# Optimization experiments

Measured on AMD Instinct MI355X. Metric: run time of the kernel, lower is better.

## Reference

```python
import jax, jax.numpy as jnp
import numpy as np

N = 131072
MUL = 64  # multiplicity of each irrep in x
FAN_IN = 128  # 2*MUL input channels per output irrep block
INV_SQRT_FAN = float(1.0 / np.sqrt(FAN_IN))
INV_SQRT3 = float(1.0 / np.sqrt(3.0))


def setup_inputs() -> dict:
    key = jax.random.key(0)
    k1, k2, k3, k4 = jax.random.split(key, 4)
    x = jax.random.normal(k1, (N, MUL + MUL * 3), dtype=jnp.float32)   # 64x0e + 64x1o
    y = jax.random.normal(k2, (N, 1 + 3), dtype=jnp.float32)           # 1x0e + 1x1o
    W0 = jax.random.normal(k3, (FAN_IN, 2 * MUL), dtype=jnp.float32)   # 0e block: 128 -> (64 gates + 64 scalars)
    b0 = jnp.zeros((2 * MUL,), dtype=jnp.float32)                      # bias only on scalars (0e)
    W1 = jax.random.normal(k4, (FAN_IN, MUL), dtype=jnp.float32)       # 1o block: 128 -> 64
    return {"x": x, "y": y, "W0": W0, "b0": b0, "W1": W1}


def reference(x, y, W0, b0, W1):
    # unpack irreps: x = 64x0e + 64x1o ; y = 1x0e + 1x1o
    x0 = x[:, :MUL]                       # [N, 64]
    x1 = x[:, MUL:].reshape(-1, MUL, 3)   # [N, 64, 3]
    y0 = y[:, :1]                         # [N, 1]
    y1 = y[:, 1:]                         # [N, 3]
    # Clebsch-Gordan tensor product (component normalization):
    #   0e x 0e -> 0e : x0 * y0
    #   1o x 1o -> 0e : dot(x1, y1)/sqrt(3)
    #   0e x 1o -> 1o : x0 * y1
    #   1o x 0e -> 1o : x1 * y0
    # (1e/2e paths are dropped by the Linear to 128x0e + 64x1o)
    tp0 = jnp.concatenate(
        [x0 * y0, jnp.einsum("nci,ni->nc", x1, y1) * INV_SQRT3], axis=-1
    )  # [N, 128] of 0e
    tp1 = jnp.concatenate(
        [x0[:, :, None] * y1[:, None, :], x1 * y0[:, :, None]], axis=1
    )  # [N, 128, 3] of 1o
    # irrep-wise Linear (element normalization => scale 1/sqrt(fan_in); bias on scalars)
    s = tp0 @ W0 * INV_SQRT_FAN + b0                      # [N, 128]: 64 gates + 64 scalars
    v = jnp.einsum("nci,co->noi", tp1, W1) * INV_SQRT_FAN  # [N, 64, 3]
    # gate: gelu on even scalars, sigmoid gates multiply the vectors
    gates = jax.nn.sigmoid(s[:, :MUL])
    scalars = jax.nn.gelu(s[:, MUL:])
    vec = (gates[:, :, None] * v).reshape(-1, MUL * 3)
    return jnp.concatenate([scalars, vec], axis=-1)  # [N, 256] = 64x0e + 64x1o
```

## Files before the change

### kernel.cpp

```cpp
#include <hip/hip_runtime.h>
#include <cstdint>

#define TPB 256

static constexpr float INV_SQRT_FAN = 0.08838834764831845f;
static constexpr float INV_SQRT3_C  = 0.5773502691896258f;

typedef _Float16 f16x4v __attribute__((ext_vector_type(4)));
typedef float f32x4 __attribute__((ext_vector_type(4)));

__device__ __align__(16) uint16_t g_wf[24576];

__device__ __forceinline__ uint16_t f2h(float f) {
  union { _Float16 h; uint16_t u; } cv;
  cv.h = (_Float16)f;
  return cv.u;
}
__device__ __forceinline__ uint32_t pk2(float a, float b) {
  return (uint32_t)f2h(a) | ((uint32_t)f2h(b) << 16);
}

__global__ void prep_kernel(const float* __restrict__ W0,
                            const float* __restrict__ W1) {
  int id = blockIdx.x * TPB + threadIdx.x;
  if (id < 16384) {
    int k = id >> 7, n = id & 127;
    g_wf[n * 128 + k] = f2h(W0[id]);
  } else {
    int i2 = id - 16384;
    int k = i2 >> 6, o = i2 & 63;
    g_wf[16384 + o * 128 + k] = f2h(W1[i2]);
  }
}

#define MFMA16H(a, b, c) __builtin_amdgcn_mfma_f32_16x16x16f16((a), (b), (c), 0, 0, 0)

__global__ __launch_bounds__(256, 4) void tplg_mfma(
    const float* __restrict__ x, const float* __restrict__ y,
    const float* __restrict__ b0, float* __restrict__ out) {
  __shared__ uint16_t lds16[18688];
  float* ldsf = (float*)lds16;
  float* s_stage = ldsf + 4096;
  float* v_stage = ldsf + 6208;

  const int t = threadIdx.x;
  const long rowBase = (long)blockIdx.x * 16;

  {
    const int u = t & 15;
    const int r = t >> 4;
    const float* xr = x + (rowBase + r) * 256;
    const float4 x0 = *(const float4*)(xr + 4 * u);
    const float4 aa = *(const float4*)(xr + 64 + 12 * u);
    const float4 bb = *(const float4*)(xr + 64 + 12 * u + 4);
    const float4 cc = *(const float4*)(xr + 64 + 12 * u + 8);
    const float4 yv = *(const float4*)(y + (rowBase + r) * 4);
    const float y0 = yv.x, y1 = yv.y, y2 = yv.z, y3 = yv.w;
    const float t0x = aa.x, t0y = aa.y, t0z = aa.z;
    const float t1x = aa.w, t1y = bb.x, t1z = bb.y;
    const float t2x = bb.z, t2y = bb.w, t2z = cc.x;
    const float t3x = cc.y, t3y = cc.z, t3z = cc.w;
    const int base = r * 512;
    const int us = u ^ r;
    *(uint2*)(lds16 + base + us * 4) =
        make_uint2(pk2(x0.x * y0, x0.y * y0), pk2(x0.z * y0, x0.w * y0));
    const float d0 = (t0x * y1 + t0y * y2 + t0z * y3) * INV_SQRT3_C;
    const float d1 = (t1x * y1 + t1y * y2 + t1z * y3) * INV_SQRT3_C;
    const float d2 = (t2x * y1 + t2y * y2 + t2z * y3) * INV_SQRT3_C;
    const float d3 = (t3x * y1 + t3y * y2 + t3z * y3) * INV_SQRT3_C;
    *(uint2*)(lds16 + base + (16 + us) * 4) = make_uint2(pk2(d0, d1), pk2(d2, d3));
    *(uint2*)(lds16 + base + (32 + us) * 4) =
        make_uint2(pk2(x0.x * y1, x0.y * y1), pk2(x0.z * y1, x0.w * y1));
    *(uint2*)(lds16 + base + (48 + us) * 4) =
        make_uint2(pk2(t0x * y0, t1x * y0), pk2(t2x * y0, t3x * y0));
    *(uint2*)(lds16 + base + (64 + us) * 4) =
        make_uint2(pk2(x0.x * y2, x0.y * y2), pk2(x0.z * y2, x0.w * y2));
    *(uint2*)(lds16 + base + (80 + us) * 4) =
        make_uint2(pk2(t0y * y0, t1y * y0), pk2(t2y * y0, t3y * y0));
    *(uint2*)(lds16 + base + (96 + us) * 4) =
        make_uint2(pk2(x0.x * y3, x0.y * y3), pk2(x0.z * y3, x0.w * y3));
    *(uint2*)(lds16 + base + (112 + us) * 4) =
        make_uint2(pk2(t0z * y0, t1z * y0), pk2(t2z * y0, t3z * y0));
  }
  __syncthreads();

  {
    const int wave = t >> 6;
    const int lane = t & 63;
    const int g = lane >> 4;
    const int q = lane & 15;
    const f32x4 zf = {0.f, 0.f, 0.f, 0.f};

    if (wave < 2) {
      const int nb = wave * 64;
      f32x4 p[4] = {zf, zf, zf, zf};
      const uint16_t* tpr = lds16 + q * 512;
      #pragma unroll
      for (int m2 = 0; m2 < 8; ++m2) {
        const f16x4v a = *(const f16x4v*)(tpr + ((m2 * 4 + g) ^ q) * 4);
        #pragma unroll
        for (int nt = 0; nt < 4; ++nt) {
          const f16x4v b =
              *(const f16x4v*)(g_wf + (nb + nt * 16 + q) * 128 + m2 * 16 + g * 4);
          p[nt] = MFMA16H(a, b, p[nt]);
        }
      }
      #pragma unroll
      for (int nt = 0; nt < 4; ++nt)
        #pragma unroll
        for (int j = 0; j < 4; ++j)
          s_stage[(g * 4 + j) * 132 + nb + nt * 16 + q] = p[nt][j];
    } else {
      const int ob = (wave - 2) * 32;
      f32x4 acc[2][3] = {{zf, zf, zf}, {zf, zf, zf}};
      #pragma unroll
      for (int m2 = 0; m2 < 8; ++m2) {
        f16x4v av[3];
        #pragma unroll
        for (int i = 0; i < 3; ++i)
          av[i] = *(const f16x4v*)(lds16 + q * 512 +
                                   (((1 + i) * 32 + m2 * 4 + g) ^ q) * 4);
        #pragma unroll
        for (int nt = 0; nt < 2; ++nt) {
          const f16x4v b = *(const f16x4v*)(g_wf + 16384 +
                                            (ob + nt * 16 + q) * 128 + m2 * 16 + g * 4);
          #pragma unroll
          for (int i = 0; i < 3; ++i) acc[nt][i] = MFMA16H(av[i], b, acc[nt][i]);
        }
      }
      #pragma unroll
      for (int nt = 0; nt < 2; ++nt)
        #pragma unroll
        for (int i = 0; i < 3; ++i)
          #pragma unroll
          for (int j = 0; j < 4; ++j)
            v_stage[(g * 4 + j) * 196 + (ob + nt * 16 + q) * 3 + i] = acc[nt][i][j];
    }
  }
  __syncthreads();

  const int r = t >> 4, w = t & 15;
  float sacc[8], vacc[12];
  #pragma unroll
  for (int n = 0; n < 8; ++n) sacc[n] = s_stage[r * 132 + 8 * w + n];
  #pragma unroll
  for (int o4 = 0; o4 < 4; ++o4)
    #pragma unroll
    for (int i = 0; i < 3; ++i)
      vacc[o4 * 3 + i] = v_stage[r * 196 + (4 * w + o4) * 3 + i];
  __syncthreads();

  float* gatep = ldsf;
  float* stg   = ldsf + 1024;
  if (w < 8) {
    #pragma unroll
    for (int n = 0; n < 8; ++n) {
      const int col = 8 * w + n;
      const float s = sacc[n] * INV_SQRT_FAN + b0[col];
      gatep[r * 64 + col] = __builtin_amdgcn_rcpf(1.0f + __expf(-s));
    }
  } else {
    #pragma unroll
    for (int n = 0; n < 8; ++n) {
      const int col = 8 * w + n;
      const float s = sacc[n] * INV_SQRT_FAN + b0[col];
      const float u3 = s * s * s;
      const float ua = 0.7978845608028654f * (s + 0.044715f * u3);
      const float e = __expf(2.0f * ua);
      const float th = 1.0f - 2.0f * __builtin_amdgcn_rcpf(e + 1.0f);
      stg[r * 256 + (col - 64)] = 0.5f * s * (1.0f + th);
    }
  }
  __syncthreads();
  #pragma unroll
  for (int o4 = 0; o4 < 4; ++o4) {
    const int o = 4 * w + o4;
    const float gq = gatep[r * 64 + o];
    #pragma unroll
    for (int i = 0; i < 3; ++i) {
      stg[r * 256 + 64 + o * 3 + i] = gq * vacc[o4 * 3 + i] * INV_SQRT_FAN;
    }
  }
  __syncthreads();

  const float4* s4 = (const float4*)stg;
  float4* o4p = (float4*)(out + rowBase * 256);
  #pragma unroll
  for (int i = 0; i < 4; ++i) o4p[i * 256 + t] = s4[i * 256 + t];
}

extern "C" void kernel_launch(void* const* d_in, const int* in_sizes, int n_in,
                              void* d_out, int out_size, void* d_ws, size_t ws_size,
                              hipStream_t stream) {
  const float* x  = (const float*)d_in[0];
  const float* y  = (const float*)d_in[1];
  const float* W0 = (const float*)d_in[2];
  const float* b0 = (const float*)d_in[3];
  const float* W1 = (const float*)d_in[4];
  float* out = (float*)d_out;
  (void)d_ws; (void)ws_size;

  const int rows = in_sizes[0] / 256;
  prep_kernel<<<24576 / TPB, TPB, 0, stream>>>(W0, W1);
  tplg_mfma<<<rows / 16, TPB, 0, stream>>>(x, y, b0, out);
}
```

Before: 299.5 us.

## Apply gate epilogue in MFMA registers and write outputs directly to global

The epilogue now runs directly on the MFMA accumulators. Wave 0 computes sigmoid gates into a small LDS buffer, wave 1 applies GELU and writes the scalars straight to global memory, and waves 2-3 read the gates and write gated vectors straight to global. This removes the s/v staging buffers, two barriers and the coalesced float4 store pass. LDS use drops enough to raise the occupancy hint from 4 to 7 blocks. The cost is scattered, uncoalesced scalar stores (stride-3 vector writes) in place of contiguous float4 stores, which may waste write bandwidth.

```diff
diff --git a/kernel.cpp b/kernel.cpp
--- a/kernel.cpp
+++ b/kernel.cpp
@@ -35,13 +35,11 @@
 
 #define MFMA16H(a, b, c) __builtin_amdgcn_mfma_f32_16x16x16f16((a), (b), (c), 0, 0, 0)
 
-__global__ __launch_bounds__(256, 4) void tplg_mfma(
+__global__ __launch_bounds__(256, 7) void tplg_mfma(
     const float* __restrict__ x, const float* __restrict__ y,
     const float* __restrict__ b0, float* __restrict__ out) {
-  __shared__ uint16_t lds16[18688];
-  float* ldsf = (float*)lds16;
-  float* s_stage = ldsf + 4096;
-  float* v_stage = ldsf + 6208;
+  __shared__ uint16_t lds16[10368];
+  float* gatesf = (float*)(lds16 + 8192);
 
   const int t = threadIdx.x;
   const long rowBase = (long)blockIdx.x * 16;
@@ -84,109 +82,95 @@
   }
   __syncthreads();
 
-  {
-    const int wave = t >> 6;
-    const int lane = t & 63;
-    const int g = lane >> 4;
-    const int q = lane & 15;
-    const f32x4 zf = {0.f, 0.f, 0.f, 0.f};
+  const int wave = t >> 6;
+  const int lane = t & 63;
+  const int g = lane >> 4;
+  const int q = lane & 15;
+  const f32x4 zf = {0.f, 0.f, 0.f, 0.f};
 
-    if (wave < 2) {
-      const int nb = wave * 64;
-      f32x4 p[4] = {zf, zf, zf, zf};
-      const uint16_t* tpr = lds16 + q * 512;
+  f32x4 acc[2][3];
+
+  if (wave < 2) {
+    const int nb = wave * 64;
+    f32x4 p[4] = {zf, zf, zf, zf};
+    const uint16_t* tpr = lds16 + q * 512;
+    #pragma unroll
+    for (int m2 = 0; m2 < 8; ++m2) {
+      const f16x4v a = *(const f16x4v*)(tpr + ((m2 * 4 + g) ^ q) * 4);
       #pragma unroll
-      for (int m2 = 0; m2 < 8; ++m2) {
-        const f16x4v a = *(const f16x4v*)(tpr + ((m2 * 4 + g) ^ q) * 4);
+      for (int nt = 0; nt < 4; ++nt) {
+        const f16x4v b =
+            *(const f16x4v*)(g_wf + (nb + nt * 16 + q) * 128 + m2 * 16 + g * 4);
+        p[nt] = MFMA16H(a, b, p[nt]);
+      }
+    }
+    if (wave == 0) {
+      #pragma unroll
+      for (int nt = 0; nt < 4; ++nt) {
+        const int col = nt * 16 + q;
+        const float bc = b0[col];
         #pragma unroll
-        for (int nt = 0; nt < 4; ++nt) {
-          const f16x4v b =
-              *(const f16x4v*)(g_wf + (nb + nt * 16 + q) * 128 + m2 * 16 + g * 4);
-          p[nt] = MFMA16H(a, b, p[nt]);
+        for (int j = 0; j < 4; ++j) {
+          const float s = p[nt][j] * INV_SQRT_FAN + bc;
+          gatesf[(g * 4 + j) * 68 + col] = __builtin_amdgcn_rcpf(1.0f + __expf(-s));
         }
       }
+    } else {
       #pragma unroll
-      for (int nt = 0; nt < 4; ++nt)
+      for (int nt = 0; nt < 4; ++nt) {
+        const int col = nt * 16 + q;
+        const float bc = b0[64 + col];
         #pragma unroll
-        for (int j = 0; j < 4; ++j)
-          s_stage[(g * 4 + j) * 132 + nb + nt * 16 + q] = p[nt][j];
-    } else {
-      const int ob = (wave - 2) * 32;
-      f32x4 acc[2][3] = {{zf, zf, zf}, {zf, zf, zf}};
-      #pragma unroll
-      for (int m2 = 0; m2 < 8; ++m2) {
-        f16x4v av[3];
-        #pragma unroll
-        for (int i = 0; i < 3; ++i)
-          av[i] = *(const f16x4v*)(lds16 + q * 512 +
-                                   (((1 + i) * 32 + m2 * 4 + g) ^ q) * 4);
-        #pragma unroll
-        for (int nt = 0; nt < 2; ++nt) {
-          const f16x4v b = *(const f16x4v*)(g_wf + 16384 +
-                                            (ob + nt * 16 + q) * 128 + m2 * 16 + g * 4);
-          #pragma unroll
-          for (int i = 0; i < 3; ++i) acc[nt][i] = MFMA16H(av[i], b, acc[nt][i]);
+        for (int j = 0; j < 4; ++j) {
+          const float s = p[nt][j] * INV_SQRT_FAN + bc;
+          const float u3 = s * s * s;
+          const float ua = 0.7978845608028654f * (s + 0.044715f * u3);
+          const float e = __expf(2.0f * ua);
+          const float th = 1.0f - 2.0f * __builtin_amdgcn_rcpf(e + 1.0f);
+          out[(rowBase + g * 4 + j) * 256 + col] = 0.5f * s * (1.0f + th);
         }
       }
+    }
+  } else {
+    const int ob = (wave - 2) * 32;
+    #pragma unroll
+    for (int nt = 0; nt < 2; ++nt)
       #pragma unroll
-      for (int nt = 0; nt < 2; ++nt)
+      for (int i = 0; i < 3; ++i) acc[nt][i] = zf;
+    #pragma unroll
+    for (int m2 = 0; m2 < 8; ++m2) {
+      f16x4v av[3];
+      #pragma unroll
+      for (int i = 0; i < 3; ++i)
+        av[i] = *(const f16x4v*)(lds16 + q * 512 +
+                                 (((1 + i) * 32 + m2 * 4 + g) ^ q) * 4);
+      #pragma unroll
+      for (int nt = 0; nt < 2; ++nt) {
+        const f16x4v b = *(const f16x4v*)(g_wf + 16384 +
+                                          (ob + nt * 16 + q) * 128 + m2 * 16 + g * 4);
         #pragma unroll
-        for (int i = 0; i < 3; ++i)
-          #pragma unroll
-          for (int j = 0; j < 4; ++j)
-            v_stage[(g * 4 + j) * 196 + (ob + nt * 16 + q) * 3 + i] = acc[nt][i][j];
+        for (int i = 0; i < 3; ++i) acc[nt][i] = MFMA16H(av[i], b, acc[nt][i]);
+      }
     }
   }
   __syncthreads();
 
-  const int r = t >> 4, w = t & 15;
-  float sacc[8], vacc[12];
-  #pragma unroll
-  for (int n = 0; n < 8; ++n) sacc[n] = s_stage[r * 132 + 8 * w + n];
-  #pragma unroll
-  for (int o4 = 0; o4 < 4; ++o4)
+  if (wave >= 2) {
+    const int ob = (wave - 2) * 32;
     #pragma unroll
-    for (int i = 0; i < 3; ++i)
-      vacc[o4 * 3 + i] = v_stage[r * 196 + (4 * w + o4) * 3 + i];
-  __syncthreads();
-
-  float* gatep = ldsf;
-  float* stg   = ldsf + 1024;
-  if (w < 8) {
-    #pragma unroll
-    for (int n = 0; n < 8; ++n) {
-      const int col = 8 * w + n;
-      const float s = sacc[n] * INV_SQRT_FAN + b0[col];
-      gatep[r * 64 + col] = __builtin_amdgcn_rcpf(1.0f + __expf(-s));
-    }
-  } else {
-    #pragma unroll
-    for (int n = 0; n < 8; ++n) {
-      const int col = 8 * w + n;
-      const float s = sacc[n] * INV_SQRT_FAN + b0[col];
-      const float u3 = s * s * s;
-      const float ua = 0.7978845608028654f * (s + 0.044715f * u3);
-      const float e = __expf(2.0f * ua);
-      const float th = 1.0f - 2.0f * __builtin_amdgcn_rcpf(e + 1.0f);
-      stg[r * 256 + (col - 64)] = 0.5f * s * (1.0f + th);
+    for (int nt = 0; nt < 2; ++nt) {
+      const int o = ob + nt * 16 + q;
+      #pragma unroll
+      for (int j = 0; j < 4; ++j) {
+        const int rr = g * 4 + j;
+        const float gq = gatesf[rr * 68 + o] * INV_SQRT_FAN;
+        float* op = out + (rowBase + rr) * 256 + 64 + o * 3;
+        op[0] = gq * acc[nt][0][j];
+        op[1] = gq * acc[nt][1][j];
+        op[2] = gq * acc[nt][2][j];
+      }
     }
   }
-  __syncthreads();
-  #pragma unroll
-  for (int o4 = 0; o4 < 4; ++o4) {
-    const int o = 4 * w + o4;
-    const float gq = gatep[r * 64 + o];
-    #pragma unroll
-    for (int i = 0; i < 3; ++i) {
-      stg[r * 256 + 64 + o * 3 + i] = gq * vacc[o4 * 3 + i] * INV_SQRT_FAN;
-    }
-  }
-  __syncthreads();
-
-  const float4* s4 = (const float4*)stg;
-  float4* o4p = (float4*)(out + rowBase * 256);
-  #pragma unroll
-  for (int i = 0; i < 4; ++i) o4p[i * 256 + t] = s4[i * 256 + t];
 }
 
 extern "C" void kernel_launch(void* const* d_in, const int* in_sizes, int n_in,
```

New measurement: 300.1 us. About the same (+0.2%).
